# Kernel optimization log

Measured on AMD Instinct MI355X. Metric: run time of the kernel, lower is better.

Reference implementation:

```python
import jax, jax.numpy as jnp
import numpy as np

K = 3
STRIDE = 1
PAD = 1


def _conv2d(x, w, b):
    y = jax.lax.conv_general_dilated(
        x, w, window_strides=(STRIDE, STRIDE),
        padding=[(PAD, PAD), (PAD, PAD)],
        dimension_numbers=("NCHW", "OIHW", "NCHW"))
    return y + b[None, :, None, None]


def _bilinear_sample(xb, py, px):
    # xb: [C, H, W]; py, px: [K2, Ho, Wo] float sample coords
    C, H, W = xb.shape
    y0 = jnp.floor(py)
    x0 = jnp.floor(px)
    ay = py - y0  # frac weights
    ax = px - x0
    out = jnp.zeros((C,) + py.shape, dtype=xb.dtype)
    corners = [
        (y0, x0, (1.0 - ay) * (1.0 - ax)),
        (y0, x0 + 1.0, (1.0 - ay) * ax),
        (y0 + 1.0, x0, ay * (1.0 - ax)),
        (y0 + 1.0, x0 + 1.0, ay * ax),
    ]
    for yc, xc, wgt in corners:
        valid = (yc >= 0) & (yc < H) & (xc >= 0) & (xc < W)
        yi = jnp.clip(yc, 0, H - 1).astype(jnp.int32)
        xi = jnp.clip(xc, 0, W - 1).astype(jnp.int32)
        g = xb[:, yi, xi]  # [C, K2, Ho, Wo]
        out = out + g * (wgt * valid.astype(xb.dtype))[None]
    return out


def _deform_forward(x, weight, bias, p_weight, p_bias):
    B, Cin, H, W = x.shape
    Cout = weight.shape[0]
    K2 = K * K
    # offset / mask prediction conv
    pout = _conv2d(x, p_weight, p_bias)  # [B, 3*K2, Ho, Wo]
    o1, o2, m = jnp.split(pout, 3, axis=1)
    offset = jnp.concatenate([o1, o2], axis=1)  # [B, 2*K2, Ho, Wo]
    mask = jax.nn.sigmoid(m)  # [B, K2, Ho, Wo]
    Ho, Wo = mask.shape[2], mask.shape[3]
    # torchvision layout: channel 2k = dy_k, 2k+1 = dx_k
    off = offset.reshape(B, K2, 2, Ho, Wo)
    dy, dx = off[:, :, 0], off[:, :, 1]  # [B, K2, Ho, Wo]
    ki = (jnp.arange(K2) // K).astype(x.dtype)  # kernel row
    kj = (jnp.arange(K2) % K).astype(x.dtype)   # kernel col
    base_y = jnp.arange(Ho, dtype=x.dtype) * STRIDE - PAD  # [Ho]
    base_x = jnp.arange(Wo, dtype=x.dtype) * STRIDE - PAD  # [Wo]
    py = base_y[None, None, :, None] + ki[None, :, None, None] + dy
    px = base_x[None, None, None, :] + kj[None, :, None, None] + dx
    sampled = jax.vmap(_bilinear_sample)(x, py, px)  # [B, Cin, K2, Ho, Wo]
    sampled = sampled * mask[:, None]
    w = weight.reshape(Cout, Cin, K2)
    out = jnp.einsum('bckhw,ock->bohw', sampled, w) + bias[None, :, None, None]
    return out


def setup_inputs() -> dict:
    key = jax.random.key(0)
    k1, k2, k3 = jax.random.split(key, 3)
    B, Cin, Cout, H, W = 4, 256, 256, 64, 64
    x = jax.random.normal(k1, (B, Cin, H, W), dtype=jnp.float32)
    fan_in = Cin * K * K
    weight = jax.random.normal(k2, (Cout, Cin, K, K), dtype=jnp.float32) / np.sqrt(fan_in)
    bias = jnp.zeros((Cout,), dtype=jnp.float32)
    # small random offset/mask predictor (zero-init in the original; randomized
    # here so the deformable sampling path is exercised)
    p_weight = jax.random.normal(k3, (3 * K * K, Cin, K, K), dtype=jnp.float32) * 0.02
    p_bias = jnp.zeros((3 * K * K,), dtype=jnp.float32)
    return {"x": x, "weight": weight, "bias": bias, "p_weight": p_weight, "p_bias": p_bias}


def reference(x, weight, bias, p_weight, p_bias):
    return _deform_forward(x, weight, bias, p_weight, p_bias)
```

## Files before the change

kernel.cpp:

```cpp
#include <hip/hip_runtime.h>
#include <stdint.h>


#define CIN 256
#define COUT 256
#define HWS 4096
#define MTOT 16384
#define KTOT 2304
#define SPLITK 8

typedef __attribute__((ext_vector_type(8))) short bf16x8;
typedef __attribute__((ext_vector_type(4))) float f32x4;

__device__ __forceinline__ unsigned short f2bf(float f) {
  unsigned int u = __float_as_uint(f);
  unsigned int r = (u + 0x7fffu + ((u >> 16) & 1u)) >> 16;
  return (unsigned short)r;
}
__device__ __forceinline__ float bf2f(unsigned short u) {
  return __uint_as_float(((unsigned int)u) << 16);
}

__device__ __forceinline__ void gload_lds16(const void* g, void* l) {
  __builtin_amdgcn_global_load_lds((const __attribute__((address_space(1))) void*)g,
                                   (__attribute__((address_space(3))) void*)l, 16, 0, 0);
}

__global__ __launch_bounds__(256) void prep_and_transpose(const float* __restrict__ x,
                                                          const float* __restrict__ w,
                                                          const float* __restrict__ pw,
                                                          unsigned short* __restrict__ xt,
                                                          unsigned short* __restrict__ WB,
                                                          unsigned short* __restrict__ PWs,
                                                          unsigned short* __restrict__ zerop) {
  __shared__ float tile[32][33];
  int bid = blockIdx.x;
  if (bid < 4096) {
    int b = bid >> 10;
    int rest = bid & 1023;
    int hw0 = (rest & 127) * 32;
    int c0 = ((rest >> 7) & 7) * 32;
    int tx = threadIdx.x & 31, ty = threadIdx.x >> 5;
    for (int i = ty; i < 32; i += 8)
      tile[i][tx] = x[(size_t)(b * CIN + c0 + i) * HWS + hw0 + tx];
    __syncthreads();
    for (int r = ty; r < 32; r += 8)
      xt[(size_t)(b * HWS + hw0 + r) * CIN + c0 + tx] = f2bf(tile[tx][r]);
  } else {
    int idx = (bid - 4096) * 256 + threadIdx.x;
    if (idx < 512)
      *(uint4*)(zerop + idx * 8) = make_uint4(0, 0, 0, 0);
    if (idx < KTOT * COUT) {
      int f = idx;
      int t_ = f & 7;
      int rest = f >> 3;
      int o = rest & 255;
      int kk = (rest >> 8) * 8 + t_;
      int k = kk >> 8, c = kk & 255;
      WB[f] = f2bf(w[o * KTOT + c * 9 + k]);
    } else {
      int f2 = idx - KTOT * COUT;
      int t_ = f2 & 7;
      int rest = f2 >> 3;
      int j = rest & 31;
      int kk = (rest >> 5) * 8 + t_;
      int k = kk >> 8, c = kk & 255;
      float v = (j < 27) ? pw[j * KTOT + c * 9 + k] : 0.0f;
      PWs[f2] = f2bf(v);
    }
  }
}

__global__ __launch_bounds__(256) void offset_conv_sk(const unsigned short* __restrict__ xt,
                                                      const unsigned short* __restrict__ PWs,
                                                      const unsigned short* __restrict__ zerop,
                                                      float* __restrict__ Pbuf) {
  __shared__ unsigned short Al[64 * 32];
  __shared__ unsigned short Bl[1024];
  int tid = threadIdx.x;
  int lane = tid & 63, wv = tid >> 6;
  int mt = (blockIdx.x & 7) * 32 + (blockIdx.x >> 3);
  int m0 = mt * 64;
  int s = blockIdx.y;
  int b = m0 >> 12;
  int hw0 = m0 & 4095;
  f32x4 acc[2] = {};

  for (int tt = 0; tt < 72 / SPLITK; ++tt) {
    int t = s * (72 / SPLITK) + tt;
    int k = t >> 3, c0 = (t & 7) * 32;
    int dyk = k / 3 - 1;
    int dxk = k % 3 - 1;
    __syncthreads();
    if (tid < 128)
      gload_lds16(PWs + (size_t)t * 1024 + tid * 8, &Bl[tid * 8]);
    {
      int r = tid >> 2;
      int hw = hw0 + r;
      int h = hw >> 6, wwp = hw & 63;
      int y = h + dyk, xx = wwp + dxk;
      bool valid = ((unsigned)y < 64u) && ((unsigned)xx < 64u);
      const unsigned short* src = valid
          ? xt + ((size_t)((b << 12) + (y << 6) + xx) << 8) + c0 + (tid & 3) * 8
          : zerop;
      gload_lds16(src, &Al[tid * 8]);
    }
    __syncthreads();
    int row = lane & 15, quad = lane >> 4;
    bf16x8 af = *(const bf16x8*)&Al[(wv * 16 + row) * 32 + quad * 8];
    for (int j = 0; j < 2; ++j) {
      bf16x8 bfr = *(const bf16x8*)&Bl[(quad * 32 + j * 16 + row) * 8];
      acc[j] = __builtin_amdgcn_mfma_f32_16x16x32_bf16(af, bfr, acc[j], 0, 0, 0);
    }
  }

  int row = lane & 15, quad = lane >> 4;
  for (int j = 0; j < 2; ++j) {
    int n = j * 16 + row;
    for (int r_ = 0; r_ < 4; ++r_) {
      int m = m0 + wv * 16 + quad * 4 + r_;
      Pbuf[((size_t)s * MTOT + m) * 32 + n] = acc[j][r_];
    }
  }
}

__global__ __launch_bounds__(256) void sample9(const unsigned short* __restrict__ xt,
                                               const float* __restrict__ Pbuf,
                                               const float* __restrict__ p_bias,
                                               unsigned short* __restrict__ A) {
  __shared__ int4 dI[4][9];
  __shared__ float4 dW[4][9];
  int tid = threadIdx.x;
  int reg = blockIdx.x & 7;
  int mb = reg * 2048 + (blockIdx.x >> 3) * 4;

  if (tid < 36) {
    int lm = tid / 9, k = tid - lm * 9;
    int m = mb + lm;
    float dy = p_bias[2 * k];
    float dx = p_bias[2 * k + 1];
    float mv = p_bias[18 + k];
#pragma unroll
    for (int s = 0; s < SPLITK; ++s) {
      const float* p = Pbuf + ((size_t)s * MTOT + m) * 32;
      dy += p[2 * k];
      dx += p[2 * k + 1];
      mv += p[18 + k];
    }
    float mk = 1.0f / (1.0f + __expf(-mv));

    int hw = m & 4095, h = hw >> 6, ww = hw & 63;
    float py = (float)(h - 1 + k / 3) + dy;
    float px = (float)(ww - 1 + k % 3) + dx;
    float y0f = floorf(py), x0f = floorf(px);
    float ay = py - y0f, ax = px - x0f;
    int y0 = (int)y0f, x0 = (int)x0f;

    float w00 = (1.f - ay) * (1.f - ax) * mk;
    float w01 = (1.f - ay) * ax * mk;
    float w10 = ay * (1.f - ax) * mk;
    float w11 = ay * ax * mk;

    float vy0 = ((unsigned)y0 < 64u) ? 1.f : 0.f;
    float vy1 = ((unsigned)(y0 + 1) < 64u) ? 1.f : 0.f;
    float vx0 = ((unsigned)x0 < 64u) ? 1.f : 0.f;
    float vx1 = ((unsigned)(x0 + 1) < 64u) ? 1.f : 0.f;
    w00 *= vy0 * vx0; w01 *= vy0 * vx1; w10 *= vy1 * vx0; w11 *= vy1 * vx1;

    int yc0 = min(max(y0, 0), 63), yc1 = min(max(y0 + 1, 0), 63);
    int xc0 = min(max(x0, 0), 63), xc1 = min(max(x0 + 1, 0), 63);

    dI[lm][k] = make_int4((yc0 * 64 + xc0) * 256, (yc0 * 64 + xc1) * 256,
                          (yc1 * 64 + xc0) * 256, (yc1 * 64 + xc1) * 256);
    dW[lm][k] = make_float4(w00, w01, w10, w11);
  }
  __syncthreads();

  int wv = tid >> 6, lane = tid & 63;
  int m = mb + wv;
  int b = m >> 12;
  const unsigned short* xtb = xt + (((size_t)b << 12) << 8);
  unsigned short* outp = A + (size_t)m * KTOT + lane * 4;

#pragma unroll
  for (int k = 0; k < 9; ++k) {
    int4 o4 = dI[wv][k];
    float4 w4 = dW[wv][k];
    ushort4 t00 = *(const ushort4*)(xtb + o4.x + 4 * lane);
    ushort4 t01 = *(const ushort4*)(xtb + o4.y + 4 * lane);
    ushort4 t10 = *(const ushort4*)(xtb + o4.z + 4 * lane);
    ushort4 t11 = *(const ushort4*)(xtb + o4.w + 4 * lane);
    float r0 = w4.x * bf2f(t00.x) + w4.y * bf2f(t01.x) + w4.z * bf2f(t10.x) + w4.w * bf2f(t11.x);
    float r1 = w4.x * bf2f(t00.y) + w4.y * bf2f(t01.y) + w4.z * bf2f(t10.y) + w4.w * bf2f(t11.y);
    float r2 = w4.x * bf2f(t00.z) + w4.y * bf2f(t01.z) + w4.z * bf2f(t10.z) + w4.w * bf2f(t11.z);
    float r3 = w4.x * bf2f(t00.w) + w4.y * bf2f(t01.w) + w4.z * bf2f(t10.w) + w4.w * bf2f(t11.w);
    ushort4 o;
    o.x = f2bf(r0); o.y = f2bf(r1); o.z = f2bf(r2); o.w = f2bf(r3);
    *(ushort4*)(outp + k * 256) = o;
  }
}

__global__ __launch_bounds__(256) void main_gemm(const unsigned short* __restrict__ Amat,
                                                 const unsigned short* __restrict__ WB,
                                                 const float* __restrict__ bias,
                                                 float* __restrict__ out) {
  __shared__ unsigned short Al[2][2][128 * 32];
  __shared__ unsigned short Bl[2][8 * 64 * 8];
  int tid = threadIdx.x;
  int lane = tid & 63, wv = tid >> 6;
  int m0 = blockIdx.x * 128;
  int n0 = blockIdx.y * 64;
  int wm = wv * 32;
  f32x4 acc[2][4] = {};

  auto stage = [&](int t, int buf) {
#pragma unroll
    for (int p = 0; p < 4; ++p) {
      int li = p * 256 + tid;
      int ks = li >> 9;
      int li2 = li & 511;
      int row = li2 >> 2, ch = li2 & 3;
      const unsigned short* src = Amat + (size_t)(m0 + row) * KTOT + t * 64 + ks * 32 + ch * 8;
      gload_lds16(src, &Al[buf][ks][li2 * 8]);
    }
#pragma unroll
    for (int p = 0; p < 2; ++p) {
      int li = p * 256 + tid;
      int kb8 = li >> 6, col = li & 63;
      const unsigned short* src = WB + ((size_t)(t * 8 + kb8) * 256 + n0 + col) * 8;
      gload_lds16(src, &Bl[buf][li * 8]);
    }
  };

  stage(0, 0);
  __syncthreads();

  int row = lane & 15, quad = lane >> 4;
  for (int t = 0; t < 36; ++t) {
    int cur = t & 1;
    if (t < 35) stage(t + 1, cur ^ 1);
#pragma unroll
    for (int ks = 0; ks < 2; ++ks) {
      bf16x8 af[2], bfr[4];
#pragma unroll
      for (int i = 0; i < 2; ++i)
        af[i] = *(const bf16x8*)&Al[cur][ks][(wm + i * 16 + row) * 32 + quad * 8];
#pragma unroll
      for (int j = 0; j < 4; ++j)
        bfr[j] = *(const bf16x8*)&Bl[cur][((ks * 4 + quad) * 64 + j * 16 + row) * 8];
#pragma unroll
      for (int i = 0; i < 2; ++i)
#pragma unroll
        for (int j = 0; j < 4; ++j)
          acc[i][j] = __builtin_amdgcn_mfma_f32_16x16x32_bf16(af[i], bfr[j], acc[i][j], 0, 0, 0);
    }
    __syncthreads();
  }

  int b = m0 >> 12, hw0 = m0 & 4095;
  for (int j = 0; j < 4; ++j) {
    int o = n0 + j * 16 + row;
    float bo = bias[o];
    for (int i = 0; i < 2; ++i) {
      int hw = hw0 + wm + i * 16 + quad * 4;
      float4 v;
      v.x = acc[i][j][0] + bo;
      v.y = acc[i][j][1] + bo;
      v.z = acc[i][j][2] + bo;
      v.w = acc[i][j][3] + bo;
      *(float4*)(out + (((size_t)(b * COUT + o)) << 12) + hw) = v;
    }
  }
}

extern "C" void kernel_launch(void* const* d_in, const int* in_sizes, int n_in,
                              void* d_out, int out_size, void* d_ws, size_t ws_size,
                              hipStream_t stream) {
  const float* x        = (const float*)d_in[0];
  const float* weight   = (const float*)d_in[1];
  const float* bias     = (const float*)d_in[2];
  const float* p_weight = (const float*)d_in[3];
  const float* p_bias   = (const float*)d_in[4];
  float* out = (float*)d_out;
  char* ws = (char*)d_ws;

  const size_t OFF_XT   = 0;
  const size_t OFF_WB   = OFF_XT + 8388608;
  const size_t OFF_PW   = OFF_WB + 1179648;
  const size_t OFF_P    = OFF_PW + 147456;
  const size_t OFF_ZP   = OFF_P + 16777216;
  const size_t OFF_A    = OFF_ZP + 8192;

  unsigned short* xt    = (unsigned short*)(ws + OFF_XT);
  unsigned short* WB    = (unsigned short*)(ws + OFF_WB);
  unsigned short* PWs   = (unsigned short*)(ws + OFF_PW);
  float* Pbuf           = (float*)(ws + OFF_P);
  unsigned short* zerop = (unsigned short*)(ws + OFF_ZP);
  unsigned short* Amat  = (unsigned short*)(ws + OFF_A);

  prep_and_transpose<<<4096 + 2592, 256, 0, stream>>>(x, weight, p_weight, xt, WB, PWs, zerop);
  offset_conv_sk<<<dim3(MTOT / 64, SPLITK), 256, 0, stream>>>(xt, PWs, zerop, Pbuf);
  sample9<<<MTOT / 4, 256, 0, stream>>>(xt, Pbuf, p_bias, Amat);
  main_gemm<<<dim3(MTOT / 128, COUT / 64), 256, 0, stream>>>(Amat, WB, bias, out);
}
```

Measured before the change: 149.4 us.

## Drop LDS staging in main GEMM and load MFMA fragments directly from global

The main GEMM no longer uses double-buffered shared memory and barriers. Each wave now reads its A and B bf16 fragments straight from global memory into registers and feeds the MFMAs, with the K loop unrolled by four. This removes LDS traffic, barrier stalls and shared-memory occupancy limits, but gives up reuse across waves: every wave re-reads the same B tile, and loads are no longer overlapped explicitly, so the kernel relies on L1/L2 caching and the compiler to hide latency.

```diff
diff --git a/kernel.cpp b/kernel.cpp
--- a/kernel.cpp
+++ b/kernel.cpp
@@ -204,63 +204,43 @@
                                                  const unsigned short* __restrict__ WB,
                                                  const float* __restrict__ bias,
                                                  float* __restrict__ out) {
-  __shared__ unsigned short Al[2][2][128 * 32];
-  __shared__ unsigned short Bl[2][8 * 64 * 8];
   int tid = threadIdx.x;
   int lane = tid & 63, wv = tid >> 6;
   int m0 = blockIdx.x * 128;
   int n0 = blockIdx.y * 64;
   int wm = wv * 32;
+  int row = lane & 15, quad = lane >> 4;
   f32x4 acc[2][4] = {};
 
-  auto stage = [&](int t, int buf) {
-#pragma unroll
-    for (int p = 0; p < 4; ++p) {
-      int li = p * 256 + tid;
-      int ks = li >> 9;
-      int li2 = li & 511;
-      int row = li2 >> 2, ch = li2 & 3;
-      const unsigned short* src = Amat + (size_t)(m0 + row) * KTOT + t * 64 + ks * 32 + ch * 8;
-      gload_lds16(src, &Al[buf][ks][li2 * 8]);
-    }
-#pragma unroll
-    for (int p = 0; p < 2; ++p) {
-      int li = p * 256 + tid;
-      int kb8 = li >> 6, col = li & 63;
-      const unsigned short* src = WB + ((size_t)(t * 8 + kb8) * 256 + n0 + col) * 8;
-      gload_lds16(src, &Bl[buf][li * 8]);
-    }
-  };
-
-  stage(0, 0);
-  __syncthreads();
-
-  int row = lane & 15, quad = lane >> 4;
-  for (int t = 0; t < 36; ++t) {
-    int cur = t & 1;
-    if (t < 35) stage(t + 1, cur ^ 1);
-#pragma unroll
-    for (int ks = 0; ks < 2; ++ks) {
-      bf16x8 af[2], bfr[4];
-#pragma unroll
-      for (int i = 0; i < 2; ++i)
-        af[i] = *(const bf16x8*)&Al[cur][ks][(wm + i * 16 + row) * 32 + quad * 8];
-#pragma unroll
-      for (int j = 0; j < 4; ++j)
-        bfr[j] = *(const bf16x8*)&Bl[cur][((ks * 4 + quad) * 64 + j * 16 + row) * 8];
-#pragma unroll
-      for (int i = 0; i < 2; ++i)
-#pragma unroll
-        for (int j = 0; j < 4; ++j)
-          acc[i][j] = __builtin_amdgcn_mfma_f32_16x16x32_bf16(af[i], bfr[j], acc[i][j], 0, 0, 0);
-    }
-    __syncthreads();
+  const unsigned short* aptr0 = Amat + (size_t)(m0 + wm + row) * KTOT + quad * 8;
+  const unsigned short* aptr1 = aptr0 + (size_t)16 * KTOT;
+  const unsigned short* bptr = WB + ((size_t)quad * 256 + n0 + row) * 8;
+
+#pragma unroll 4
+  for (int t = 0; t < 72; ++t) {
+    bf16x8 a0 = *(const bf16x8*)(aptr0 + t * 32);
+    bf16x8 a1 = *(const bf16x8*)(aptr1 + t * 32);
+    const unsigned short* bt = bptr + t * 8192;
+    bf16x8 b0 = *(const bf16x8*)(bt);
+    bf16x8 b1 = *(const bf16x8*)(bt + 128);
+    bf16x8 b2 = *(const bf16x8*)(bt + 256);
+    bf16x8 b3 = *(const bf16x8*)(bt + 384);
+    acc[0][0] = __builtin_amdgcn_mfma_f32_16x16x32_bf16(a0, b0, acc[0][0], 0, 0, 0);
+    acc[0][1] = __builtin_amdgcn_mfma_f32_16x16x32_bf16(a0, b1, acc[0][1], 0, 0, 0);
+    acc[0][2] = __builtin_amdgcn_mfma_f32_16x16x32_bf16(a0, b2, acc[0][2], 0, 0, 0);
+    acc[0][3] = __builtin_amdgcn_mfma_f32_16x16x32_bf16(a0, b3, acc[0][3], 0, 0, 0);
+    acc[1][0] = __builtin_amdgcn_mfma_f32_16x16x32_bf16(a1, b0, acc[1][0], 0, 0, 0);
+    acc[1][1] = __builtin_amdgcn_mfma_f32_16x16x32_bf16(a1, b1, acc[1][1], 0, 0, 0);
+    acc[1][2] = __builtin_amdgcn_mfma_f32_16x16x32_bf16(a1, b2, acc[1][2], 0, 0, 0);
+    acc[1][3] = __builtin_amdgcn_mfma_f32_16x16x32_bf16(a1, b3, acc[1][3], 0, 0, 0);
   }
 
   int b = m0 >> 12, hw0 = m0 & 4095;
+#pragma unroll
   for (int j = 0; j < 4; ++j) {
     int o = n0 + j * 16 + row;
     float bo = bias[o];
+#pragma unroll
     for (int i = 0; i < 2; ++i) {
       int hw = hw0 + wm + i * 16 + quad * 4;
       float4 v;
```

After: 169.2 us. 13.3% more time.
